# Optimization experiments

Measured on AMD Instinct MI355X. Metric: run time of the kernel, lower is better.

Reference implementation:

```python
import jax, jax.numpy as jnp
import numpy as np

B, S, H, L = 8, 4096, 768, 256   # batch, seq_len, hidden_size, num_lines (= line_ids.max()+1)
ATT_HID = 1024                    # attention MLP hidden dim from nn.Linear(hidden,1024)


def setup_inputs() -> dict:
    key = jax.random.key(0)
    k0, k1, k2, k3 = jax.random.split(key, 4)
    token_hidden = jax.random.normal(k0, (B, S, H), dtype=jnp.float32)
    line_ids = jax.random.randint(k1, (B, S), 0, L)  # all valid; -1 would mark invalid
    W1 = jax.random.normal(k2, (H, ATT_HID), dtype=jnp.float32) * 0.02
    b1 = jnp.zeros((ATT_HID,), jnp.float32)
    W2 = jax.random.normal(k3, (ATT_HID, 1), dtype=jnp.float32) * 0.02
    b2 = jnp.zeros((1,), jnp.float32)
    return {"token_hidden": token_hidden, "line_ids": line_ids,
            "W1": W1, "b1": b1, "W2": W2, "b2": b2}


def reference(token_hidden, line_ids, W1, b1, W2, b2):
    b, s, h = token_hidden.shape
    num_lines = L
    n_seg = b * num_lines + 1  # last segment is a dump slot for invalid (-1) tokens

    # attention scores: Linear -> tanh -> Linear, squeeze(-1)  [b, s]
    scores = (jnp.tanh(token_hidden @ W1 + b1) @ W2 + b2)[..., 0]

    valid = (line_ids >= 0).reshape(-1)                                   # [b*s]
    seg = jnp.where(line_ids >= 0,
                    jnp.arange(b)[:, None] * num_lines + line_ids,
                    b * num_lines).reshape(-1)                            # [b*s]
    s_flat = jnp.where(valid, scores.reshape(-1), -jnp.inf)

    # segment-wise stable softmax
    m = jax.ops.segment_max(s_flat, seg, num_segments=n_seg)
    m = jnp.where(jnp.isfinite(m), m, 0.0)  # empty segments -> safe 0
    e = jnp.where(valid, jnp.exp(scores.reshape(-1) - m[seg]), 0.0)
    denom = jax.ops.segment_sum(e, seg, num_segments=n_seg)
    w = e / jnp.maximum(denom[seg], 1e-20)                                # [b*s]

    # weighted sum of tokens per (batch, line) segment
    feats = jax.ops.segment_sum(token_hidden.reshape(-1, h) * w[:, None],
                                seg, num_segments=n_seg)
    line_features = feats[: b * num_lines].reshape(b, num_lines, h)

    counts = jax.ops.segment_sum(valid.astype(jnp.float32), seg, num_segments=n_seg)
    line_mask = counts[: b * num_lines].reshape(b, num_lines) > 0
    return line_features, line_mask
```

## Files before the change

kernel.cpp:

```cpp
#include <hip/hip_runtime.h>
#include <hip/hip_bf16.h>
#include <string.h>

#define M_TOK 32768
#define H_DIM 768
#define AH    1024
#define NSEG  2048
#define CAP   96

typedef __attribute__((ext_vector_type(8))) __bf16 bf16x8;
typedef __attribute__((ext_vector_type(4))) float f32x4;

__device__ __forceinline__ float tanh_fast(float x) {
  float e = __expf(2.0f * x);
  return 1.0f - 2.0f * __builtin_amdgcn_rcpf(e + 1.0f);
}

__global__ __launch_bounds__(256) void prep_kernel(
    const float* __restrict__ W1, __hip_bfloat16* __restrict__ W1t,
    const int* __restrict__ line_ids, int* __restrict__ cursor,
    int* __restrict__ order) {
  __shared__ float tile[32][33];
  if (blockIdx.x < 768) {
    int nt = blockIdx.x & 31, ktile = blockIdx.x >> 5;
    int n0 = nt * 32, k0 = ktile * 32;
    int tx = threadIdx.x & 31, ty = threadIdx.x >> 5;
    for (int r = ty; r < 32; r += 8)
      tile[r][tx] = W1[(size_t)(k0 + r) * AH + n0 + tx];
    __syncthreads();
    for (int r = ty; r < 32; r += 8)
      W1t[(size_t)(n0 + r) * H_DIM + k0 + tx] = __float2bfloat16(tile[tx][r]);
  } else {
    int t = (blockIdx.x - 768) * 256 + threadIdx.x;
    int lid = line_ids[t];
    if (lid >= 0) {
      int seg = (t >> 12) * 256 + lid;
      int pos = atomicAdd(&cursor[seg], 1);
      if (pos < CAP) order[seg * CAP + pos] = t;
    }
  }
}

__global__ __launch_bounds__(256) void attn_score_kernel(
    const float* __restrict__ Xf, const __hip_bfloat16* __restrict__ W1tg,
    const float* __restrict__ b1g, const float* __restrict__ W2g,
    float* __restrict__ scores) {
  __shared__ __align__(16) __bf16 As[128 * 32];
  __shared__ __align__(16) __bf16 Bs[128 * 32];

  const int tid = threadIdx.x;
  const int bid = blockIdx.x;
  const int xcd = bid & 7;
  const int s   = bid >> 3;
  const int m0  = (xcd * 32 + (s >> 3)) * 128;
  const int n0  = (s & 7) * 128;
  const int lane = tid & 63;
  const int wave = tid >> 6;
  const int wm   = (wave >> 1) * 64;
  const int wn   = (wave & 1) * 64;
  const int q8   = (lane >> 4) * 8;
  const int ml   = lane & 15;

  const __bf16* W = (const __bf16*)W1tg;

  const int rowoff = tid >> 2;
  const int colk   = (tid & 3) * 8;

  f32x4 acc[4][4];
#pragma unroll
  for (int i = 0; i < 4; i++)
#pragma unroll
    for (int j = 0; j < 4; j++) acc[i][j] = (f32x4)0.f;

  for (int kt = 0; kt < H_DIM; kt += 32) {
#pragma unroll
    for (int r = 0; r < 2; ++r) {
      const __bf16* gb = W + (size_t)(n0 + r * 64 + rowoff) * H_DIM + kt + colk;
      __builtin_amdgcn_global_load_lds(
          (const __attribute__((address_space(1))) void*)gb,
          (__attribute__((address_space(3))) void*)&Bs[(r * 256 + tid) * 8],
          16, 0, 0);
      const float* ga = Xf + (size_t)(m0 + r * 64 + rowoff) * H_DIM + kt + colk;
      float4 v0 = *(const float4*)ga;
      float4 v1 = *(const float4*)(ga + 4);
      __hip_bfloat16 h[8] = {
          __float2bfloat16(v0.x), __float2bfloat16(v0.y),
          __float2bfloat16(v0.z), __float2bfloat16(v0.w),
          __float2bfloat16(v1.x), __float2bfloat16(v1.y),
          __float2bfloat16(v1.z), __float2bfloat16(v1.w)};
      memcpy(&As[(r * 256 + tid) * 8], h, 16);
    }
    __syncthreads();

    bf16x8 af[4], bf[4];
#pragma unroll
    for (int i = 0; i < 4; i++)
      af[i] = *(const bf16x8*)&As[(wm + i * 16 + ml) * 32 + q8];
#pragma unroll
    for (int j = 0; j < 4; j++)
      bf[j] = *(const bf16x8*)&Bs[(wn + j * 16 + ml) * 32 + q8];

#pragma unroll
    for (int i = 0; i < 4; i++)
#pragma unroll
      for (int j = 0; j < 4; j++)
        acc[i][j] = __builtin_amdgcn_mfma_f32_16x16x32_bf16(af[i], bf[j],
                                                            acc[i][j], 0, 0, 0);
    __syncthreads();
  }

  float b1v[4], w2v[4];
#pragma unroll
  for (int j = 0; j < 4; j++) {
    int n = n0 + wn + j * 16 + ml;
    b1v[j] = b1g[n];
    w2v[j] = W2g[n];
  }
  const int q4 = (lane >> 4) * 4;
#pragma unroll
  for (int i = 0; i < 4; i++) {
#pragma unroll
    for (int p = 0; p < 4; p++) {
      float t = 0.f;
#pragma unroll
      for (int j = 0; j < 4; j++)
        t += tanh_fast(acc[i][j][p] + b1v[j]) * w2v[j];
      t += __shfl_xor(t, 1);
      t += __shfl_xor(t, 2);
      t += __shfl_xor(t, 4);
      t += __shfl_xor(t, 8);
      if (ml == 0) atomicAdd(&scores[m0 + wm + i * 16 + q4 + p], t);
    }
  }
}

__global__ __launch_bounds__(256) void aggregate_kernel(
    const float4* __restrict__ X4, const float* __restrict__ scores,
    const int* __restrict__ cursor, const int* __restrict__ order,
    float4* __restrict__ out4, float* __restrict__ out_mask) {
  __shared__ float sw[CAP];
  __shared__ int   sidx[CAP];
  __shared__ float wred[4];
  const int seg = blockIdx.x;
  const int tid = threadIdx.x;
  int cnt = cursor[seg];
  if (cnt > CAP) cnt = CAP;
  if (tid == 0) out_mask[seg] = cnt > 0 ? 1.f : 0.f;
  if (cnt == 0) {
    if (tid < H_DIM / 4)
      out4[(size_t)seg * (H_DIM / 4) + tid] = make_float4(0.f, 0.f, 0.f, 0.f);
    return;
  }
  const int lane = tid & 63, wave = tid >> 6;
  float lmax = -3.4e38f;
  if (tid < cnt) {
    int idx = order[seg * CAP + tid];
    sidx[tid] = idx;
    float sc = scores[idx];
    sw[tid] = sc;
    lmax = sc;
  }
#pragma unroll
  for (int d = 1; d < 64; d <<= 1) lmax = fmaxf(lmax, __shfl_xor(lmax, d));
  if (lane == 0) wred[wave] = lmax;
  __syncthreads();
  float m = fmaxf(fmaxf(wred[0], wred[1]), fmaxf(wred[2], wred[3]));
  float lsum = 0.f;
  if (tid < cnt) {
    float e = __expf(sw[tid] - m);
    sw[tid] = e;
    lsum = e;
  }
#pragma unroll
  for (int d = 1; d < 64; d <<= 1) lsum += __shfl_xor(lsum, d);
  __syncthreads();
  if (lane == 0) wred[wave] = lsum;
  __syncthreads();
  float denom = wred[0] + wred[1] + wred[2] + wred[3];
  float inv = __builtin_amdgcn_rcpf(fmaxf(denom, 1e-20f));
  if (tid < cnt) sw[tid] *= inv;
  __syncthreads();
  if (tid < H_DIM / 4) {
    const float4* base = X4 + tid;
    float4 acc = make_float4(0.f, 0.f, 0.f, 0.f);
    int t = 0;
    for (; t + 4 <= cnt; t += 4) {
      int i0 = sidx[t], i1 = sidx[t + 1], i2 = sidx[t + 2], i3 = sidx[t + 3];
      float4 v0 = base[(size_t)i0 * (H_DIM / 4)];
      float4 v1 = base[(size_t)i1 * (H_DIM / 4)];
      float4 v2 = base[(size_t)i2 * (H_DIM / 4)];
      float4 v3 = base[(size_t)i3 * (H_DIM / 4)];
      float w0 = sw[t], w1 = sw[t + 1], w2 = sw[t + 2], w3 = sw[t + 3];
      acc.x += w0 * v0.x + w1 * v1.x + w2 * v2.x + w3 * v3.x;
      acc.y += w0 * v0.y + w1 * v1.y + w2 * v2.y + w3 * v3.y;
      acc.z += w0 * v0.z + w1 * v1.z + w2 * v2.z + w3 * v3.z;
      acc.w += w0 * v0.w + w1 * v1.w + w2 * v2.w + w3 * v3.w;
    }
    for (; t < cnt; ++t) {
      float w = sw[t];
      float4 v = base[(size_t)sidx[t] * (H_DIM / 4)];
      acc.x += w * v.x; acc.y += w * v.y; acc.z += w * v.z; acc.w += w * v.w;
    }
    out4[(size_t)seg * (H_DIM / 4) + tid] = acc;
  }
}

extern "C" void kernel_launch(void* const* d_in, const int* in_sizes, int n_in,
                              void* d_out, int out_size, void* d_ws, size_t ws_size,
                              hipStream_t stream) {
  const float* X        = (const float*)d_in[0];
  const int*   line_ids = (const int*)d_in[1];
  const float* W1       = (const float*)d_in[2];
  const float* b1       = (const float*)d_in[3];
  const float* W2       = (const float*)d_in[4];

  char* p = (char*)d_ws;
  __hip_bfloat16* W1t = (__hip_bfloat16*)p;  p += 1572864;
  float* scores  = (float*)p;                p += 131072;
  int*   cursor  = (int*)p;                  p += 8192;
  int*   order   = (int*)p;                  p += (size_t)NSEG * CAP * 4;

  float* out_feats = (float*)d_out;
  float* out_mask  = out_feats + (size_t)NSEG * H_DIM;

  hipMemsetAsync(scores, 0, 131072 + 8192, stream);

  prep_kernel<<<768 + M_TOK / 256, 256, 0, stream>>>(W1, W1t, line_ids,
                                                     cursor, order);
  attn_score_kernel<<<2048, 256, 0, stream>>>(X, W1t, b1, W2, scores);
  aggregate_kernel<<<NSEG, 256, 0, stream>>>((const float4*)X, scores, cursor,
                                             order, (float4*)out_feats, out_mask);
}
```

Before: 271.4 us.

## Pre-convert token hidden to bf16 once and reuse in GEMM and aggregation

Adds a conversion pass in the prep kernel that writes the whole fp32 token_hidden as a bf16 copy into workspace. The score GEMM then loads the A tile with direct global-to-LDS loads instead of loading fp32 and converting inside the K loop. The aggregation gather also reads the bf16 copy, halving its bytes. In exchange there is an extra full read of X plus a bf16 write, and the weighted sum now uses bf16-rounded token values, which lowers output precision.

```diff
diff --git a/kernel.cpp b/kernel.cpp
--- a/kernel.cpp
+++ b/kernel.cpp
@@ -7,6 +7,7 @@
 #define AH    1024
 #define NSEG  2048
 #define CAP   96
+#define CONV_BLOCKS 12288
 
 typedef __attribute__((ext_vector_type(8))) __bf16 bf16x8;
 typedef __attribute__((ext_vector_type(4))) float f32x4;
@@ -16,10 +17,18 @@
   return 1.0f - 2.0f * __builtin_amdgcn_rcpf(e + 1.0f);
 }
 
+__device__ __forceinline__ float bf2f(unsigned short u) {
+  unsigned int v = (unsigned int)u << 16;
+  float f;
+  memcpy(&f, &v, 4);
+  return f;
+}
+
 __global__ __launch_bounds__(256) void prep_kernel(
     const float* __restrict__ W1, __hip_bfloat16* __restrict__ W1t,
     const int* __restrict__ line_ids, int* __restrict__ cursor,
-    int* __restrict__ order) {
+    int* __restrict__ order, const float4* __restrict__ X4,
+    uint4* __restrict__ Xb4) {
   __shared__ float tile[32][33];
   if (blockIdx.x < 768) {
     int nt = blockIdx.x & 31, ktile = blockIdx.x >> 5;
@@ -30,7 +39,7 @@
     __syncthreads();
     for (int r = ty; r < 32; r += 8)
       W1t[(size_t)(n0 + r) * H_DIM + k0 + tx] = __float2bfloat16(tile[tx][r]);
-  } else {
+  } else if (blockIdx.x < 896) {
     int t = (blockIdx.x - 768) * 256 + threadIdx.x;
     int lid = line_ids[t];
     if (lid >= 0) {
@@ -38,13 +47,25 @@
       int pos = atomicAdd(&cursor[seg], 1);
       if (pos < CAP) order[seg * CAP + pos] = t;
     }
+  } else {
+    int i = (blockIdx.x - 896) * 256 + threadIdx.x;
+    float4 v0 = X4[i * 2];
+    float4 v1 = X4[i * 2 + 1];
+    __hip_bfloat16 h[8] = {
+        __float2bfloat16(v0.x), __float2bfloat16(v0.y),
+        __float2bfloat16(v0.z), __float2bfloat16(v0.w),
+        __float2bfloat16(v1.x), __float2bfloat16(v1.y),
+        __float2bfloat16(v1.z), __float2bfloat16(v1.w)};
+    uint4 p;
+    memcpy(&p, h, 16);
+    Xb4[i] = p;
   }
 }
 
 __global__ __launch_bounds__(256) void attn_score_kernel(
-    const float* __restrict__ Xf, const __hip_bfloat16* __restrict__ W1tg,
-    const float* __restrict__ b1g, const float* __restrict__ W2g,
-    float* __restrict__ scores) {
+    const __hip_bfloat16* __restrict__ Xbg,
+    const __hip_bfloat16* __restrict__ W1tg, const float* __restrict__ b1g,
+    const float* __restrict__ W2g, float* __restrict__ scores) {
   __shared__ __align__(16) __bf16 As[128 * 32];
   __shared__ __align__(16) __bf16 Bs[128 * 32];
 
@@ -61,7 +82,8 @@
   const int q8   = (lane >> 4) * 8;
   const int ml   = lane & 15;
 
-  const __bf16* W = (const __bf16*)W1tg;
+  const __bf16* Xb = (const __bf16*)Xbg;
+  const __bf16* W  = (const __bf16*)W1tg;
 
   const int rowoff = tid >> 2;
   const int colk   = (tid & 3) * 8;
@@ -75,20 +97,16 @@
   for (int kt = 0; kt < H_DIM; kt += 32) {
 #pragma unroll
     for (int r = 0; r < 2; ++r) {
+      const __bf16* ga = Xb + (size_t)(m0 + r * 64 + rowoff) * H_DIM + kt + colk;
+      __builtin_amdgcn_global_load_lds(
+          (const __attribute__((address_space(1))) void*)ga,
+          (__attribute__((address_space(3))) void*)&As[(r * 256 + tid) * 8],
+          16, 0, 0);
       const __bf16* gb = W + (size_t)(n0 + r * 64 + rowoff) * H_DIM + kt + colk;
       __builtin_amdgcn_global_load_lds(
           (const __attribute__((address_space(1))) void*)gb,
           (__attribute__((address_space(3))) void*)&Bs[(r * 256 + tid) * 8],
           16, 0, 0);
-      const float* ga = Xf + (size_t)(m0 + r * 64 + rowoff) * H_DIM + kt + colk;
-      float4 v0 = *(const float4*)ga;
-      float4 v1 = *(const float4*)(ga + 4);
-      __hip_bfloat16 h[8] = {
-          __float2bfloat16(v0.x), __float2bfloat16(v0.y),
-          __float2bfloat16(v0.z), __float2bfloat16(v0.w),
-          __float2bfloat16(v1.x), __float2bfloat16(v1.y),
-          __float2bfloat16(v1.z), __float2bfloat16(v1.w)};
-      memcpy(&As[(r * 256 + tid) * 8], h, 16);
     }
     __syncthreads();
 
@@ -135,7 +153,7 @@
 }
 
 __global__ __launch_bounds__(256) void aggregate_kernel(
-    const float4* __restrict__ X4, const float* __restrict__ scores,
+    const ushort* __restrict__ Xb, const float* __restrict__ scores,
     const int* __restrict__ cursor, const int* __restrict__ order,
     float4* __restrict__ out4, float* __restrict__ out_mask) {
   __shared__ float sw[CAP];
@@ -181,25 +199,25 @@
   if (tid < cnt) sw[tid] *= inv;
   __syncthreads();
   if (tid < H_DIM / 4) {
-    const float4* base = X4 + tid;
+    const ushort4* base = (const ushort4*)Xb + tid;
     float4 acc = make_float4(0.f, 0.f, 0.f, 0.f);
     int t = 0;
     for (; t + 4 <= cnt; t += 4) {
-      int i0 = sidx[t], i1 = sidx[t + 1], i2 = sidx[t + 2], i3 = sidx[t + 3];
-      float4 v0 = base[(size_t)i0 * (H_DIM / 4)];
-      float4 v1 = base[(size_t)i1 * (H_DIM / 4)];
-      float4 v2 = base[(size_t)i2 * (H_DIM / 4)];
-      float4 v3 = base[(size_t)i3 * (H_DIM / 4)];
+      ushort4 u0 = base[(size_t)sidx[t]     * (H_DIM / 4)];
+      ushort4 u1 = base[(size_t)sidx[t + 1] * (H_DIM / 4)];
+      ushort4 u2 = base[(size_t)sidx[t + 2] * (H_DIM / 4)];
+      ushort4 u3 = base[(size_t)sidx[t + 3] * (H_DIM / 4)];
       float w0 = sw[t], w1 = sw[t + 1], w2 = sw[t + 2], w3 = sw[t + 3];
-      acc.x += w0 * v0.x + w1 * v1.x + w2 * v2.x + w3 * v3.x;
-      acc.y += w0 * v0.y + w1 * v1.y + w2 * v2.y + w3 * v3.y;
-      acc.z += w0 * v0.z + w1 * v1.z + w2 * v2.z + w3 * v3.z;
-      acc.w += w0 * v0.w + w1 * v1.w + w2 * v2.w + w3 * v3.w;
+      acc.x += w0 * bf2f(u0.x) + w1 * bf2f(u1.x) + w2 * bf2f(u2.x) + w3 * bf2f(u3.x);
+      acc.y += w0 * bf2f(u0.y) + w1 * bf2f(u1.y) + w2 * bf2f(u2.y) + w3 * bf2f(u3.y);
+      acc.z += w0 * bf2f(u0.z) + w1 * bf2f(u1.z) + w2 * bf2f(u2.z) + w3 * bf2f(u3.z);
+      acc.w += w0 * bf2f(u0.w) + w1 * bf2f(u1.w) + w2 * bf2f(u2.w) + w3 * bf2f(u3.w);
     }
     for (; t < cnt; ++t) {
+      ushort4 u = base[(size_t)sidx[t] * (H_DIM / 4)];
       float w = sw[t];
-      float4 v = base[(size_t)sidx[t] * (H_DIM / 4)];
-      acc.x += w * v.x; acc.y += w * v.y; acc.z += w * v.z; acc.w += w * v.w;
+      acc.x += w * bf2f(u.x); acc.y += w * bf2f(u.y);
+      acc.z += w * bf2f(u.z); acc.w += w * bf2f(u.w);
     }
     out4[(size_t)seg * (H_DIM / 4) + tid] = acc;
   }
@@ -215,6 +233,7 @@
   const float* W2       = (const float*)d_in[4];
 
   char* p = (char*)d_ws;
+  __hip_bfloat16* Xb  = (__hip_bfloat16*)p;  p += (size_t)M_TOK * H_DIM * 2;
   __hip_bfloat16* W1t = (__hip_bfloat16*)p;  p += 1572864;
   float* scores  = (float*)p;                p += 131072;
   int*   cursor  = (int*)p;                  p += 8192;
@@ -225,9 +244,9 @@
 
   hipMemsetAsync(scores, 0, 131072 + 8192, stream);
 
-  prep_kernel<<<768 + M_TOK / 256, 256, 0, stream>>>(W1, W1t, line_ids,
-                                                     cursor, order);
-  attn_score_kernel<<<2048, 256, 0, stream>>>(X, W1t, b1, W2, scores);
-  aggregate_kernel<<<NSEG, 256, 0, stream>>>((const float4*)X, scores, cursor,
+  prep_kernel<<<896 + CONV_BLOCKS, 256, 0, stream>>>(
+      W1, W1t, line_ids, cursor, order, (const float4*)X, (uint4*)Xb);
+  attn_score_kernel<<<2048, 256, 0, stream>>>(Xb, W1t, b1, W2, scores);
+  aggregate_kernel<<<NSEG, 256, 0, stream>>>((const ushort*)Xb, scores, cursor,
                                              order, (float4*)out_feats, out_mask);
 }
```

Result: faster. 252.9 us (-6.8%).
